# Performance work log

Hardware: AMD Instinct MI355X
Metric: run time of the kernel (lower is better)

The kernel has to match this reference:

```python
import jax, jax.numpy as jnp
import numpy as np

B = 16384          # batch
NB = 2             # n_boxes
NC = 20            # n_classes
LC = 5.0           # lambda_coord
LN = 0.5           # lambda_noobj
IOU_EPS = 1e-6
P_EPS = 1e-7       # BCE log clamp (torch clamps log at -100; eps-clip is equivalent in effect)


def setup_inputs() -> dict:
    key = jax.random.key(0)
    k1, k2, k3, k4 = jax.random.split(key, 4)
    # predictions: uniform [0,1) so sqrt() of w/h and BCE on confidence are well-defined,
    # matching the assumption of the original (sigmoid-style outputs)
    y_pred = jax.random.uniform(k1, (B, 7, 7, 5 * NB + NC), dtype=jnp.float32)
    # ground-truth feature map as produced by transform_to_yolo:
    # [x_frac, y_frac, w, h, objectness(0/1), class_label], zeros in empty cells
    conf = (jax.random.uniform(k2, (B, 7, 7)) < 0.08).astype(jnp.float32)  # ~4 objects/img
    coords = jax.random.uniform(k3, (B, 7, 7, 4), dtype=jnp.float32)
    labels = jax.random.randint(k4, (B, 7, 7), 0, NC).astype(jnp.float32)
    y_true = jnp.concatenate([coords, conf[..., None], labels[..., None]], axis=-1) * conf[..., None]
    return {"y_pred": y_pred, "y_true": y_true}


def _iou(b1, b2):
    # b1: [B,7,7,NB,>=4], b2: [B,7,7,1,4] (cxcywh) -> iou [B,7,7,NB]
    b1x1 = b1[..., 0] - b1[..., 2] / 2
    b1x2 = b1[..., 0] + b1[..., 2] / 2
    b1y1 = b1[..., 1] - b1[..., 3] / 2
    b1y2 = b1[..., 1] + b1[..., 3] / 2
    b2x1 = b2[..., 0] - b2[..., 2] / 2
    b2x2 = b2[..., 0] + b2[..., 2] / 2
    b2y1 = b2[..., 1] - b2[..., 3] / 2
    b2y2 = b2[..., 1] + b2[..., 3] / 2
    inter = jnp.clip(jnp.minimum(b1x2, b2x2) - jnp.maximum(b1x1, b2x1), 0) * \
            jnp.clip(jnp.minimum(b1y2, b2y2) - jnp.maximum(b1y1, b2y1), 0)
    union = b1[..., 2] * b1[..., 3] + b2[..., 2] * b2[..., 3] - inter
    return inter / (union + IOU_EPS)


def reference(y_pred, y_true):
    boxes = y_pred[..., :5 * NB].reshape(y_pred.shape[:-1] + (NB, 5))  # [B,7,7,NB,5]
    ious = _iou(boxes, y_true[..., None, :4])                          # [B,7,7,NB]
    best = jnp.argmax(ious, axis=-1)                                   # [B,7,7]
    tb = jnp.take_along_axis(boxes, best[..., None, None], axis=3)[..., 0, :]  # [B,7,7,5]

    obj = (y_true[..., 4] != 0).astype(y_pred.dtype)
    noobj = 1.0 - obj
    n_obj = jnp.sum(obj)
    n_noobj = jnp.sum(noobj)

    def mmse(a, b, m, n):  # masked-mean MSE, matching F.mse_loss over masked elements
        return jnp.sum(m * (a - b) ** 2) / n

    def mbce(p, t, m, n):
        pc = jnp.clip(p, P_EPS, 1.0 - P_EPS)
        return jnp.sum(m * -(t * jnp.log(pc) + (1.0 - t) * jnp.log1p(-pc))) / n

    coord = LC * (mmse(tb[..., 0], y_true[..., 0], obj, n_obj) +
                  mmse(tb[..., 1], y_true[..., 1], obj, n_obj))
    # NOTE: original compares sqrt(pred_h) against sqrt(y_true[...,2]) (index-2 twice); kept faithfully.
    size = LC * (mmse(jnp.sqrt(tb[..., 2]), jnp.sqrt(y_true[..., 2]), obj, n_obj) +
                 mmse(jnp.sqrt(tb[..., 3]), jnp.sqrt(y_true[..., 2]), obj, n_obj))
    conf_l = mbce(tb[..., 4], y_true[..., 4], obj, n_obj) + \
             LN * mbce(tb[..., 4], y_true[..., 4], noobj, n_noobj)

    logits = y_pred[..., 5 * NB:]                       # [B,7,7,NC]
    logp = jax.nn.log_softmax(logits, axis=-1)
    lbl = y_true[..., 5].astype(jnp.int32)
    nll = -jnp.take_along_axis(logp, lbl[..., None], axis=-1)[..., 0]
    ce = jnp.sum(obj * nll) / n_obj

    return coord + size + conf_l + ce
```

## Files before the change

kernel.cpp:

```cpp
#include <hip/hip_runtime.h>


#define CELLS  (16384 * 49)
#define TILE   256
#define NTILES (CELLS / TILE)
#define NCH    30
#define NTR    6
#define LCOORD 5.0f
#define LNOOBJ 0.5f

__device__ __forceinline__ float iou_one(float x, float y, float w, float h,
                                         float t0, float t1, float t2, float t3) {
    float b1x1 = x - w * 0.5f, b1x2 = x + w * 0.5f;
    float b1y1 = y - h * 0.5f, b1y2 = y + h * 0.5f;
    float b2x1 = t0 - t2 * 0.5f, b2x2 = t0 + t2 * 0.5f;
    float b2y1 = t1 - t3 * 0.5f, b2y2 = t1 + t3 * 0.5f;
    float iw = fmaxf(fminf(b1x2, b2x2) - fmaxf(b1x1, b2x1), 0.0f);
    float ih = fmaxf(fminf(b1y2, b2y2) - fmaxf(b1y1, b2y1), 0.0f);
    float inter = iw * ih;
    float uni = w * h + t2 * t3 - inter;
    return inter / (uni + 1e-6f);
}

__global__ __launch_bounds__(256) void yolo_main(const float* __restrict__ yp,
                                                 const float* __restrict__ yt,
                                                 float* __restrict__ ws,
                                                 int ntiles_per_block_grid) {
    __shared__ float sp[TILE * NCH];
    __shared__ float st[TILE * NTR];
    __shared__ float red[4][8];

    const int tid = threadIdx.x;
    float v[6] = {0.f, 0.f, 0.f, 0.f, 0.f, 0.f};

    for (int tile = blockIdx.x; tile < NTILES; tile += gridDim.x) {
        const float4* gp4 = (const float4*)(yp + (size_t)tile * TILE * NCH);
        float4* sp4 = (float4*)sp;
        #pragma unroll
        for (int i = tid; i < TILE * NCH / 4; i += 256) sp4[i] = gp4[i];
        const float4* gt4 = (const float4*)(yt + (size_t)tile * TILE * NTR);
        float4* st4 = (float4*)st;
        for (int i = tid; i < TILE * NTR / 4; i += 256) st4[i] = gt4[i];
        __syncthreads();

        const float* p = sp + tid * NCH;
        const float* t = st + tid * NTR;
        float t0 = t[0], t1 = t[1], t2 = t[2], t3 = t[3], t4 = t[4];
        int lbl = (int)t[5];

        float iou0 = iou_one(p[0], p[1], p[2], p[3], t0, t1, t2, t3);
        float iou1 = iou_one(p[5], p[6], p[7], p[8], t0, t1, t2, t3);
        int base = (iou1 > iou0) ? 5 : 0;
        float tb0 = p[base + 0], tb1 = p[base + 1], tb2 = p[base + 2];
        float tb3 = p[base + 3], tb4 = p[base + 4];

        float obj = (t4 != 0.0f) ? 1.0f : 0.0f;
        float noobj = 1.0f - obj;

        float dx = tb0 - t0, dy = tb1 - t1;
        float a0 = obj * (dx * dx + dy * dy);

        float s2 = sqrtf(t2);
        float d2 = sqrtf(tb2) - s2;
        float d3 = sqrtf(tb3) - s2;
        float a1 = obj * (d2 * d2 + d3 * d3);

        float pc = fminf(fmaxf(tb4, 1e-7f), 1.0f - 1e-7f);
        float bce = -(t4 * logf(pc) + (1.0f - t4) * log1pf(-pc));
        float a2 = obj * bce;
        float a3 = noobj * bce;

        float m = p[10];
        #pragma unroll
        for (int k = 11; k < 30; ++k) m = fmaxf(m, p[k]);
        float se = 0.0f;
        #pragma unroll
        for (int k = 10; k < 30; ++k) se += expf(p[k] - m);
        float nll = logf(se) + m - p[10 + lbl];
        float a4 = obj * nll;

        v[0] += a0; v[1] += a1; v[2] += a2; v[3] += a3; v[4] += a4; v[5] += obj;
        __syncthreads();
    }

    #pragma unroll
    for (int j = 0; j < 6; ++j) {
        #pragma unroll
        for (int off = 32; off > 0; off >>= 1)
            v[j] += __shfl_down(v[j], off, 64);
    }
    const int wave = tid >> 6, lane = tid & 63;
    if (lane == 0) {
        #pragma unroll
        for (int j = 0; j < 6; ++j) red[wave][j] = v[j];
    }
    __syncthreads();
    if (tid == 0) {
        float* dst = ws + (size_t)blockIdx.x * 8;
        #pragma unroll
        for (int j = 0; j < 6; ++j)
            dst[j] = red[0][j] + red[1][j] + red[2][j] + red[3][j];
    }
}

__global__ __launch_bounds__(256) void yolo_final(const float* __restrict__ ws,
                                                  float* __restrict__ out,
                                                  int nblocks) {
    __shared__ float red[4][8];
    const int tid = threadIdx.x;
    float v[6] = {0.f, 0.f, 0.f, 0.f, 0.f, 0.f};
    for (int i = tid; i < nblocks; i += 256) {
        const float* src = ws + (size_t)i * 8;
        #pragma unroll
        for (int j = 0; j < 6; ++j) v[j] += src[j];
    }
    #pragma unroll
    for (int j = 0; j < 6; ++j) {
        #pragma unroll
        for (int off = 32; off > 0; off >>= 1)
            v[j] += __shfl_down(v[j], off, 64);
    }
    const int wave = tid >> 6, lane = tid & 63;
    if (lane == 0) {
        #pragma unroll
        for (int j = 0; j < 6; ++j) red[wave][j] = v[j];
    }
    __syncthreads();
    if (tid == 0) {
        float a[6];
        #pragma unroll
        for (int j = 0; j < 6; ++j)
            a[j] = red[0][j] + red[1][j] + red[2][j] + red[3][j];
        float n_obj = a[5];
        float n_noobj = (float)CELLS - n_obj;
        float loss = (LCOORD * (a[0] + a[1]) + a[2] + a[4]) / n_obj
                   + LNOOBJ * a[3] / n_noobj;
        out[0] = loss;
    }
}

extern "C" void kernel_launch(void* const* d_in, const int* in_sizes, int n_in,
                              void* d_out, int out_size, void* d_ws, size_t ws_size,
                              hipStream_t stream) {
    const float* yp = (const float*)d_in[0];
    const float* yt = (const float*)d_in[1];
    float* out = (float*)d_out;
    float* ws = (float*)d_ws;

    int nblocks = NTILES;
    size_t need = (size_t)nblocks * 8 * sizeof(float);
    if (ws_size < need) {
        nblocks = (int)(ws_size / (8 * sizeof(float)));
        if (nblocks > NTILES) nblocks = NTILES;
        if (nblocks < 1) nblocks = 1;
    }

    yolo_main<<<nblocks, 256, 0, stream>>>(yp, yt, ws, nblocks);
    yolo_final<<<1, 256, 0, stream>>>(ws, out, nblocks);
}
```

Baseline: 169.8 us.

## Fuse final reduction via last-block atomic and use direct global-to-LDS loads

```diff
diff --git a/kernel.cpp b/kernel.cpp
--- a/kernel.cpp
+++ b/kernel.cpp
@@ -8,6 +8,7 @@
 #define NTR    6
 #define LCOORD 5.0f
 #define LNOOBJ 0.5f
+#define PART_OFF 16
 
 __device__ __forceinline__ float iou_one(float x, float y, float w, float h,
                                          float t0, float t1, float t2, float t3) {
@@ -22,25 +23,45 @@
     return inter / (uni + 1e-6f);
 }
 
-__global__ __launch_bounds__(256) void yolo_main(const float* __restrict__ yp,
-                                                 const float* __restrict__ yt,
-                                                 float* __restrict__ ws,
-                                                 int ntiles_per_block_grid) {
+__global__ __launch_bounds__(256) void yolo_fused(const float* __restrict__ yp,
+                                                  const float* __restrict__ yt,
+                                                  float* __restrict__ ws,
+                                                  float* __restrict__ out,
+                                                  int nblocks) {
     __shared__ float sp[TILE * NCH];
     __shared__ float st[TILE * NTR];
     __shared__ float red[4][8];
+    __shared__ int is_last;
 
-    const int tid = threadIdx.x;
+    const int tid  = threadIdx.x;
+    const int wave = tid >> 6, lane = tid & 63;
     float v[6] = {0.f, 0.f, 0.f, 0.f, 0.f, 0.f};
 
     for (int tile = blockIdx.x; tile < NTILES; tile += gridDim.x) {
         const float4* gp4 = (const float4*)(yp + (size_t)tile * TILE * NCH);
+        const float4* gt4 = (const float4*)(yt + (size_t)tile * TILE * NTR);
         float4* sp4 = (float4*)sp;
+        float4* st4 = (float4*)st;
         #pragma unroll
-        for (int i = tid; i < TILE * NCH / 4; i += 256) sp4[i] = gp4[i];
-        const float4* gt4 = (const float4*)(yt + (size_t)tile * TILE * NTR);
-        float4* st4 = (float4*)st;
-        for (int i = tid; i < TILE * NTR / 4; i += 256) st4[i] = gt4[i];
+        for (int k = 0; k < 8; ++k) {
+            int i = k * 256 + tid;
+            if (i < TILE * NCH / 4) {
+                int base = k * 256 + wave * 64;
+                __builtin_amdgcn_global_load_lds(
+                    (const __attribute__((address_space(1))) void*)(gp4 + i),
+                    (__attribute__((address_space(3))) void*)(sp4 + base), 16, 0, 0);
+            }
+        }
+        #pragma unroll
+        for (int k = 0; k < 2; ++k) {
+            int i = k * 256 + tid;
+            if (i < TILE * NTR / 4) {
+                int base = k * 256 + wave * 64;
+                __builtin_amdgcn_global_load_lds(
+                    (const __attribute__((address_space(1))) void*)(gt4 + i),
+                    (__attribute__((address_space(3))) void*)(st4 + base), 16, 0, 0);
+            }
+        }
         __syncthreads();
 
         const float* p = sp + tid * NCH;
@@ -89,53 +110,50 @@
         for (int off = 32; off > 0; off >>= 1)
             v[j] += __shfl_down(v[j], off, 64);
     }
-    const int wave = tid >> 6, lane = tid & 63;
     if (lane == 0) {
         #pragma unroll
         for (int j = 0; j < 6; ++j) red[wave][j] = v[j];
     }
     __syncthreads();
     if (tid == 0) {
-        float* dst = ws + (size_t)blockIdx.x * 8;
+        float* dst = ws + PART_OFF + (size_t)blockIdx.x * 8;
         #pragma unroll
         for (int j = 0; j < 6; ++j)
             dst[j] = red[0][j] + red[1][j] + red[2][j] + red[3][j];
-    }
-}
-
-__global__ __launch_bounds__(256) void yolo_final(const float* __restrict__ ws,
-                                                  float* __restrict__ out,
-                                                  int nblocks) {
-    __shared__ float red[4][8];
-    const int tid = threadIdx.x;
-    float v[6] = {0.f, 0.f, 0.f, 0.f, 0.f, 0.f};
-    for (int i = tid; i < nblocks; i += 256) {
-        const float* src = ws + (size_t)i * 8;
-        #pragma unroll
-        for (int j = 0; j < 6; ++j) v[j] += src[j];
-    }
-    #pragma unroll
-    for (int j = 0; j < 6; ++j) {
-        #pragma unroll
-        for (int off = 32; off > 0; off >>= 1)
-            v[j] += __shfl_down(v[j], off, 64);
-    }
-    const int wave = tid >> 6, lane = tid & 63;
-    if (lane == 0) {
-        #pragma unroll
-        for (int j = 0; j < 6; ++j) red[wave][j] = v[j];
+        unsigned old = __hip_atomic_fetch_add((unsigned*)ws, 1u,
+                                              __ATOMIC_ACQ_REL, __HIP_MEMORY_SCOPE_AGENT);
+        is_last = (old == (unsigned)(nblocks - 1)) ? 1 : 0;
     }
     __syncthreads();
-    if (tid == 0) {
-        float a[6];
+
+    if (is_last) {
+        float f[6] = {0.f, 0.f, 0.f, 0.f, 0.f, 0.f};
+        for (int i = tid; i < nblocks; i += 256) {
+            const float* src = ws + PART_OFF + (size_t)i * 8;
+            #pragma unroll
+            for (int j = 0; j < 6; ++j) f[j] += src[j];
+        }
         #pragma unroll
-        for (int j = 0; j < 6; ++j)
-            a[j] = red[0][j] + red[1][j] + red[2][j] + red[3][j];
-        float n_obj = a[5];
-        float n_noobj = (float)CELLS - n_obj;
-        float loss = (LCOORD * (a[0] + a[1]) + a[2] + a[4]) / n_obj
+        for (int j = 0; j < 6; ++j) {
+            #pragma unroll
+            for (int off = 32; off > 0; off >>= 1)
+                f[j] += __shfl_down(f[j], off, 64);
+        }
+        if (lane == 0) {
+            #pragma unroll
+            for (int j = 0; j < 6; ++j) red[wave][j] = f[j];
+        }
+        __syncthreads();
+        if (tid == 0) {
+            float a[6];
+            #pragma unroll
+            for (int j = 0; j < 6; ++j)
+                a[j] = red[0][j] + red[1][j] + red[2][j] + red[3][j];
+            float n_obj = a[5];
+            float n_noobj = (float)CELLS - n_obj;
+            out[0] = (LCOORD * (a[0] + a[1]) + a[2] + a[4]) / n_obj
                    + LNOOBJ * a[3] / n_noobj;
-        out[0] = loss;
+        }
     }
 }
 
@@ -148,13 +166,13 @@
     float* ws = (float*)d_ws;
 
     int nblocks = NTILES;
-    size_t need = (size_t)nblocks * 8 * sizeof(float);
+    size_t need = 64 + (size_t)nblocks * 8 * sizeof(float);
     if (ws_size < need) {
-        nblocks = (int)(ws_size / (8 * sizeof(float)));
+        nblocks = (int)((ws_size - 64) / (8 * sizeof(float)));
         if (nblocks > NTILES) nblocks = NTILES;
         if (nblocks < 1) nblocks = 1;
     }
 
-    yolo_main<<<nblocks, 256, 0, stream>>>(yp, yt, ws, nblocks);
-    yolo_final<<<1, 256, 0, stream>>>(ws, out, nblocks);
+    hipMemsetAsync(ws, 0, 64, stream);
+    yolo_fused<<<nblocks, 256, 0, stream>>>(yp, yt, ws, out, nblocks);
 }
```

Result: slower. 283.7 us (+67.1%).

## Use persistent 784-block grid with register prefetch of the next tile

Applied to the files above, without the earlier changes.

```diff
diff --git a/kernel.cpp b/kernel.cpp
--- a/kernel.cpp
+++ b/kernel.cpp
@@ -1,13 +1,15 @@
 #include <hip/hip_runtime.h>
 
 
-#define CELLS  (16384 * 49)
-#define TILE   256
-#define NTILES (CELLS / TILE)
-#define NCH    30
-#define NTR    6
-#define LCOORD 5.0f
-#define LNOOBJ 0.5f
+#define CELLS   (16384 * 49)
+#define TILE    256
+#define NTILES  (CELLS / TILE)
+#define NBLOCKS 784
+#define TPB     4
+#define NCH     30
+#define NTR     6
+#define LCOORD  5.0f
+#define LNOOBJ  0.5f
 
 __device__ __forceinline__ float iou_one(float x, float y, float w, float h,
                                          float t0, float t1, float t2, float t3) {
@@ -24,63 +26,97 @@
 
 __global__ __launch_bounds__(256) void yolo_main(const float* __restrict__ yp,
                                                  const float* __restrict__ yt,
-                                                 float* __restrict__ ws,
-                                                 int ntiles_per_block_grid) {
+                                                 float* __restrict__ ws) {
     __shared__ float sp[TILE * NCH];
     __shared__ float st[TILE * NTR];
     __shared__ float red[4][8];
 
-    const int tid = threadIdx.x;
+    const int tid  = threadIdx.x;
+    const int wave = tid >> 6, lane = tid & 63;
+    const bool lo  = (tid < 128);
     float v[6] = {0.f, 0.f, 0.f, 0.f, 0.f, 0.f};
 
-    for (int tile = blockIdx.x; tile < NTILES; tile += gridDim.x) {
+    float4* sp4 = (float4*)sp;
+    float4* st4 = (float4*)st;
+
+    float4 pa[8], pb[2];
+    float4 qa[8], qb[2];
+
+    {
+        const int tile = blockIdx.x;
         const float4* gp4 = (const float4*)(yp + (size_t)tile * TILE * NCH);
-        float4* sp4 = (float4*)sp;
+        const float4* gt4 = (const float4*)(yt + (size_t)tile * TILE * NTR);
         #pragma unroll
-        for (int i = tid; i < TILE * NCH / 4; i += 256) sp4[i] = gp4[i];
-        const float4* gt4 = (const float4*)(yt + (size_t)tile * TILE * NTR);
-        float4* st4 = (float4*)st;
-        for (int i = tid; i < TILE * NTR / 4; i += 256) st4[i] = gt4[i];
+        for (int s = 0; s < 7; ++s) pa[s] = gp4[s * 256 + tid];
+        if (lo) pa[7] = gp4[7 * 256 + tid];
+        pb[0] = gt4[tid];
+        if (lo) pb[1] = gt4[256 + tid];
+    }
+
+    #pragma unroll
+    for (int k = 0; k < TPB; ++k) {
+        #pragma unroll
+        for (int s = 0; s < 7; ++s) sp4[s * 256 + tid] = pa[s];
+        if (lo) sp4[7 * 256 + tid] = pa[7];
+        st4[tid] = pb[0];
+        if (lo) st4[256 + tid] = pb[1];
         __syncthreads();
 
-        const float* p = sp + tid * NCH;
-        const float* t = st + tid * NTR;
-        float t0 = t[0], t1 = t[1], t2 = t[2], t3 = t[3], t4 = t[4];
-        int lbl = (int)t[5];
+        if (k < TPB - 1) {
+            const int ntile = blockIdx.x + (k + 1) * NBLOCKS;
+            const float4* gp4 = (const float4*)(yp + (size_t)ntile * TILE * NCH);
+            const float4* gt4 = (const float4*)(yt + (size_t)ntile * TILE * NTR);
+            #pragma unroll
+            for (int s = 0; s < 7; ++s) qa[s] = gp4[s * 256 + tid];
+            if (lo) qa[7] = gp4[7 * 256 + tid];
+            qb[0] = gt4[tid];
+            if (lo) qb[1] = gt4[256 + tid];
+        }
 
-        float iou0 = iou_one(p[0], p[1], p[2], p[3], t0, t1, t2, t3);
-        float iou1 = iou_one(p[5], p[6], p[7], p[8], t0, t1, t2, t3);
-        int base = (iou1 > iou0) ? 5 : 0;
-        float tb0 = p[base + 0], tb1 = p[base + 1], tb2 = p[base + 2];
-        float tb3 = p[base + 3], tb4 = p[base + 4];
+        {
+            const float* p = sp + tid * NCH;
+            const float* t = st + tid * NTR;
+            float t0 = t[0], t1 = t[1], t2 = t[2], t3 = t[3], t4 = t[4];
+            int lbl = (int)t[5];
 
-        float obj = (t4 != 0.0f) ? 1.0f : 0.0f;
-        float noobj = 1.0f - obj;
+            float iou0 = iou_one(p[0], p[1], p[2], p[3], t0, t1, t2, t3);
+            float iou1 = iou_one(p[5], p[6], p[7], p[8], t0, t1, t2, t3);
+            int base = (iou1 > iou0) ? 5 : 0;
+            float tb0 = p[base + 0], tb1 = p[base + 1], tb2 = p[base + 2];
+            float tb3 = p[base + 3], tb4 = p[base + 4];
 
-        float dx = tb0 - t0, dy = tb1 - t1;
-        float a0 = obj * (dx * dx + dy * dy);
+            float obj = (t4 != 0.0f) ? 1.0f : 0.0f;
+            float noobj = 1.0f - obj;
 
-        float s2 = sqrtf(t2);
-        float d2 = sqrtf(tb2) - s2;
-        float d3 = sqrtf(tb3) - s2;
-        float a1 = obj * (d2 * d2 + d3 * d3);
+            float dx = tb0 - t0, dy = tb1 - t1;
+            float a0 = obj * (dx * dx + dy * dy);
 
-        float pc = fminf(fmaxf(tb4, 1e-7f), 1.0f - 1e-7f);
-        float bce = -(t4 * logf(pc) + (1.0f - t4) * log1pf(-pc));
-        float a2 = obj * bce;
-        float a3 = noobj * bce;
+            float s2 = sqrtf(t2);
+            float d2 = sqrtf(tb2) - s2;
+            float d3 = sqrtf(tb3) - s2;
+            float a1 = obj * (d2 * d2 + d3 * d3);
 
-        float m = p[10];
+            float pc = fminf(fmaxf(tb4, 1e-7f), 1.0f - 1e-7f);
+            float bce = -(t4 * logf(pc) + (1.0f - t4) * log1pf(-pc));
+            float a2 = obj * bce;
+            float a3 = noobj * bce;
+
+            float m = p[10];
+            #pragma unroll
+            for (int c = 11; c < 30; ++c) m = fmaxf(m, p[c]);
+            float se = 0.0f;
+            #pragma unroll
+            for (int c = 10; c < 30; ++c) se += expf(p[c] - m);
+            float nll = logf(se) + m - p[10 + lbl];
+            float a4 = obj * nll;
+
+            v[0] += a0; v[1] += a1; v[2] += a2; v[3] += a3; v[4] += a4; v[5] += obj;
+        }
+        __syncthreads();
+
         #pragma unroll
-        for (int k = 11; k < 30; ++k) m = fmaxf(m, p[k]);
-        float se = 0.0f;
-        #pragma unroll
-        for (int k = 10; k < 30; ++k) se += expf(p[k] - m);
-        float nll = logf(se) + m - p[10 + lbl];
-        float a4 = obj * nll;
-
-        v[0] += a0; v[1] += a1; v[2] += a2; v[3] += a3; v[4] += a4; v[5] += obj;
-        __syncthreads();
+        for (int s = 0; s < 8; ++s) pa[s] = qa[s];
+        pb[0] = qb[0]; pb[1] = qb[1];
     }
 
     #pragma unroll
@@ -89,7 +125,6 @@
         for (int off = 32; off > 0; off >>= 1)
             v[j] += __shfl_down(v[j], off, 64);
     }
-    const int wave = tid >> 6, lane = tid & 63;
     if (lane == 0) {
         #pragma unroll
         for (int j = 0; j < 6; ++j) red[wave][j] = v[j];
@@ -104,12 +139,11 @@
 }
 
 __global__ __launch_bounds__(256) void yolo_final(const float* __restrict__ ws,
-                                                  float* __restrict__ out,
-                                                  int nblocks) {
+                                                  float* __restrict__ out) {
     __shared__ float red[4][8];
     const int tid = threadIdx.x;
     float v[6] = {0.f, 0.f, 0.f, 0.f, 0.f, 0.f};
-    for (int i = tid; i < nblocks; i += 256) {
+    for (int i = tid; i < NBLOCKS; i += 256) {
         const float* src = ws + (size_t)i * 8;
         #pragma unroll
         for (int j = 0; j < 6; ++j) v[j] += src[j];
@@ -133,9 +167,8 @@
             a[j] = red[0][j] + red[1][j] + red[2][j] + red[3][j];
         float n_obj = a[5];
         float n_noobj = (float)CELLS - n_obj;
-        float loss = (LCOORD * (a[0] + a[1]) + a[2] + a[4]) / n_obj
-                   + LNOOBJ * a[3] / n_noobj;
-        out[0] = loss;
+        out[0] = (LCOORD * (a[0] + a[1]) + a[2] + a[4]) / n_obj
+               + LNOOBJ * a[3] / n_noobj;
     }
 }
 
@@ -147,14 +180,6 @@
     float* out = (float*)d_out;
     float* ws = (float*)d_ws;
 
-    int nblocks = NTILES;
-    size_t need = (size_t)nblocks * 8 * sizeof(float);
-    if (ws_size < need) {
-        nblocks = (int)(ws_size / (8 * sizeof(float)));
-        if (nblocks > NTILES) nblocks = NTILES;
-        if (nblocks < 1) nblocks = 1;
-    }
-
-    yolo_main<<<nblocks, 256, 0, stream>>>(yp, yt, ws, nblocks);
-    yolo_final<<<1, 256, 0, stream>>>(ws, out, nblocks);
+    yolo_main<<<NBLOCKS, 256, 0, stream>>>(yp, yt, ws);
+    yolo_final<<<1, 256, 0, stream>>>(ws, out);
 }
```

New measurement: 237.9 us. +40.1%, slower.

## Load two cells per thread directly into registers, dropping LDS staging

Applied to the files above, without the earlier changes.

```diff
diff --git a/kernel.cpp b/kernel.cpp
--- a/kernel.cpp
+++ b/kernel.cpp
@@ -1,13 +1,11 @@
 #include <hip/hip_runtime.h>
 
 
-#define CELLS  (16384 * 49)
-#define TILE   256
-#define NTILES (CELLS / TILE)
-#define NCH    30
-#define NTR    6
-#define LCOORD 5.0f
-#define LNOOBJ 0.5f
+#define CELLS    (16384 * 49)
+#define NTHREADS (CELLS / 2)
+#define NBLK     (NTHREADS / 256)
+#define LCOORD   5.0f
+#define LNOOBJ   0.5f
 
 __device__ __forceinline__ float iou_one(float x, float y, float w, float h,
                                          float t0, float t1, float t2, float t3) {
@@ -22,66 +20,86 @@
     return inter / (uni + 1e-6f);
 }
 
-__global__ __launch_bounds__(256) void yolo_main(const float* __restrict__ yp,
-                                                 const float* __restrict__ yt,
-                                                 float* __restrict__ ws,
-                                                 int ntiles_per_block_grid) {
-    __shared__ float sp[TILE * NCH];
-    __shared__ float st[TILE * NTR];
+__device__ __forceinline__ void cell_loss(const float (&p)[30], const float (&t)[6],
+                                          float (&v)[6]) {
+    float t0 = t[0], t1 = t[1], t2 = t[2], t3 = t[3], t4 = t[4];
+    int lbl = (int)t[5];
+
+    float iou0 = iou_one(p[0], p[1], p[2], p[3], t0, t1, t2, t3);
+    float iou1 = iou_one(p[5], p[6], p[7], p[8], t0, t1, t2, t3);
+    bool sel = (iou1 > iou0);
+    float tb0 = sel ? p[5] : p[0];
+    float tb1 = sel ? p[6] : p[1];
+    float tb2 = sel ? p[7] : p[2];
+    float tb3 = sel ? p[8] : p[3];
+    float tb4 = sel ? p[9] : p[4];
+
+    float obj = (t4 != 0.0f) ? 1.0f : 0.0f;
+    float noobj = 1.0f - obj;
+
+    float dx = tb0 - t0, dy = tb1 - t1;
+    float a0 = obj * (dx * dx + dy * dy);
+
+    float s2 = sqrtf(t2);
+    float d2 = sqrtf(tb2) - s2;
+    float d3 = sqrtf(tb3) - s2;
+    float a1 = obj * (d2 * d2 + d3 * d3);
+
+    float pc = fminf(fmaxf(tb4, 1e-7f), 1.0f - 1e-7f);
+    float bce = -(t4 * logf(pc) + (1.0f - t4) * log1pf(-pc));
+    float a2 = obj * bce;
+    float a3 = noobj * bce;
+
+    float m = p[10];
+    #pragma unroll
+    for (int c = 11; c < 30; ++c) m = fmaxf(m, p[c]);
+    float se = 0.0f;
+    #pragma unroll
+    for (int c = 10; c < 30; ++c) se += expf(p[c] - m);
+    float plbl = p[10];
+    #pragma unroll
+    for (int c = 1; c < 20; ++c) plbl = (lbl == c) ? p[10 + c] : plbl;
+    float nll = logf(se) + m - plbl;
+    float a4 = obj * nll;
+
+    v[0] += a0; v[1] += a1; v[2] += a2; v[3] += a3; v[4] += a4; v[5] += obj;
+}
+
+__global__ __launch_bounds__(256, 1) void yolo_main(const float4* __restrict__ yp4,
+                                                    const float4* __restrict__ yt4,
+                                                    float* __restrict__ ws) {
     __shared__ float red[4][8];
+    const int tid = threadIdx.x;
+    const int gid = blockIdx.x * 256 + tid;
 
-    const int tid = threadIdx.x;
+    const float4* gp = yp4 + (size_t)gid * 15;
+    float4 g[15];
+    #pragma unroll
+    for (int i = 0; i < 15; ++i) g[i] = gp[i];
+    const float4* gt = yt4 + (size_t)gid * 3;
+    float4 h0 = gt[0], h1 = gt[1], h2 = gt[2];
+
+    float pA[30], pB[30], tA[6], tB[6];
+    #pragma unroll
+    for (int i = 0; i < 7; ++i) {
+        pA[4 * i + 0] = g[i].x; pA[4 * i + 1] = g[i].y;
+        pA[4 * i + 2] = g[i].z; pA[4 * i + 3] = g[i].w;
+    }
+    pA[28] = g[7].x; pA[29] = g[7].y;
+    pB[0]  = g[7].z; pB[1]  = g[7].w;
+    #pragma unroll
+    for (int i = 0; i < 7; ++i) {
+        pB[2 + 4 * i + 0] = g[8 + i].x; pB[2 + 4 * i + 1] = g[8 + i].y;
+        pB[2 + 4 * i + 2] = g[8 + i].z; pB[2 + 4 * i + 3] = g[8 + i].w;
+    }
+    tA[0] = h0.x; tA[1] = h0.y; tA[2] = h0.z; tA[3] = h0.w;
+    tA[4] = h1.x; tA[5] = h1.y;
+    tB[0] = h1.z; tB[1] = h1.w;
+    tB[2] = h2.x; tB[3] = h2.y; tB[4] = h2.z; tB[5] = h2.w;
+
     float v[6] = {0.f, 0.f, 0.f, 0.f, 0.f, 0.f};
-
-    for (int tile = blockIdx.x; tile < NTILES; tile += gridDim.x) {
-        const float4* gp4 = (const float4*)(yp + (size_t)tile * TILE * NCH);
-        float4* sp4 = (float4*)sp;
-        #pragma unroll
-        for (int i = tid; i < TILE * NCH / 4; i += 256) sp4[i] = gp4[i];
-        const float4* gt4 = (const float4*)(yt + (size_t)tile * TILE * NTR);
-        float4* st4 = (float4*)st;
-        for (int i = tid; i < TILE * NTR / 4; i += 256) st4[i] = gt4[i];
-        __syncthreads();
-
-        const float* p = sp + tid * NCH;
-        const float* t = st + tid * NTR;
-        float t0 = t[0], t1 = t[1], t2 = t[2], t3 = t[3], t4 = t[4];
-        int lbl = (int)t[5];
-
-        float iou0 = iou_one(p[0], p[1], p[2], p[3], t0, t1, t2, t3);
-        float iou1 = iou_one(p[5], p[6], p[7], p[8], t0, t1, t2, t3);
-        int base = (iou1 > iou0) ? 5 : 0;
-        float tb0 = p[base + 0], tb1 = p[base + 1], tb2 = p[base + 2];
-        float tb3 = p[base + 3], tb4 = p[base + 4];
-
-        float obj = (t4 != 0.0f) ? 1.0f : 0.0f;
-        float noobj = 1.0f - obj;
-
-        float dx = tb0 - t0, dy = tb1 - t1;
-        float a0 = obj * (dx * dx + dy * dy);
-
-        float s2 = sqrtf(t2);
-        float d2 = sqrtf(tb2) - s2;
-        float d3 = sqrtf(tb3) - s2;
-        float a1 = obj * (d2 * d2 + d3 * d3);
-
-        float pc = fminf(fmaxf(tb4, 1e-7f), 1.0f - 1e-7f);
-        float bce = -(t4 * logf(pc) + (1.0f - t4) * log1pf(-pc));
-        float a2 = obj * bce;
-        float a3 = noobj * bce;
-
-        float m = p[10];
-        #pragma unroll
-        for (int k = 11; k < 30; ++k) m = fmaxf(m, p[k]);
-        float se = 0.0f;
-        #pragma unroll
-        for (int k = 10; k < 30; ++k) se += expf(p[k] - m);
-        float nll = logf(se) + m - p[10 + lbl];
-        float a4 = obj * nll;
-
-        v[0] += a0; v[1] += a1; v[2] += a2; v[3] += a3; v[4] += a4; v[5] += obj;
-        __syncthreads();
-    }
+    cell_loss(pA, tA, v);
+    cell_loss(pB, tB, v);
 
     #pragma unroll
     for (int j = 0; j < 6; ++j) {
@@ -104,12 +122,11 @@
 }
 
 __global__ __launch_bounds__(256) void yolo_final(const float* __restrict__ ws,
-                                                  float* __restrict__ out,
-                                                  int nblocks) {
+                                                  float* __restrict__ out) {
     __shared__ float red[4][8];
     const int tid = threadIdx.x;
     float v[6] = {0.f, 0.f, 0.f, 0.f, 0.f, 0.f};
-    for (int i = tid; i < nblocks; i += 256) {
+    for (int i = tid; i < NBLK; i += 256) {
         const float* src = ws + (size_t)i * 8;
         #pragma unroll
         for (int j = 0; j < 6; ++j) v[j] += src[j];
@@ -133,28 +150,19 @@
             a[j] = red[0][j] + red[1][j] + red[2][j] + red[3][j];
         float n_obj = a[5];
         float n_noobj = (float)CELLS - n_obj;
-        float loss = (LCOORD * (a[0] + a[1]) + a[2] + a[4]) / n_obj
-                   + LNOOBJ * a[3] / n_noobj;
-        out[0] = loss;
+        out[0] = (LCOORD * (a[0] + a[1]) + a[2] + a[4]) / n_obj
+               + LNOOBJ * a[3] / n_noobj;
     }
 }
 
 extern "C" void kernel_launch(void* const* d_in, const int* in_sizes, int n_in,
                               void* d_out, int out_size, void* d_ws, size_t ws_size,
                               hipStream_t stream) {
-    const float* yp = (const float*)d_in[0];
-    const float* yt = (const float*)d_in[1];
+    const float4* yp4 = (const float4*)d_in[0];
+    const float4* yt4 = (const float4*)d_in[1];
     float* out = (float*)d_out;
     float* ws = (float*)d_ws;
 
-    int nblocks = NTILES;
-    size_t need = (size_t)nblocks * 8 * sizeof(float);
-    if (ws_size < need) {
-        nblocks = (int)(ws_size / (8 * sizeof(float)));
-        if (nblocks > NTILES) nblocks = NTILES;
-        if (nblocks < 1) nblocks = 1;
-    }
-
-    yolo_main<<<nblocks, 256, 0, stream>>>(yp, yt, ws, nblocks);
-    yolo_final<<<1, 256, 0, stream>>>(ws, out, nblocks);
+    yolo_main<<<NBLK, 256, 0, stream>>>(yp4, yt4, ws);
+    yolo_final<<<1, 256, 0, stream>>>(ws, out);
 }
```

Measured after the change: 164.0 us. 1.04x faster.
